# Kernel tuning notes

Hardware: AMD Instinct MI355X
Metric: run time of the kernel (lower is better)

## Reference

```python
import jax, jax.numpy as jnp
import numpy as np

B, IN_DIM, HID, S = 131072, 8, 32, 16
ERR_THR = 0.01          # QuantumErrorCorrection.error_threshold
ENT_STRENGTH = 0.4      # config.quantum_entanglement_strength
EULER_DT = 0.1


def setup_inputs() -> dict:
    key = jax.random.key(0)
    ks = jax.random.split(key, 7)
    x = jax.random.normal(ks[0], (B, IN_DIM), dtype=jnp.float32)
    h_quantum = jax.random.normal(ks[1], (B, HID, S), dtype=jnp.float32)
    quantum_weights = jax.random.normal(ks[2], (IN_DIM, HID, S), dtype=jnp.float32) * 0.1
    recurrent_weights = jax.random.normal(ks[3], (HID, HID, S), dtype=jnp.float32) * 0.1
    base_tau = jax.random.uniform(ks[4], (HID,), dtype=jnp.float32, minval=1.0, maxval=50.0)
    syndrome_matrix = jax.random.normal(ks[5], (4, S), dtype=jnp.float32)
    correction_weights = jax.random.normal(ks[6], (4, S), dtype=jnp.float32) * 0.1
    return {"x": x, "h_quantum": h_quantum, "quantum_weights": quantum_weights,
            "recurrent_weights": recurrent_weights, "base_tau": base_tau,
            "syndrome_matrix": syndrome_matrix, "correction_weights": correction_weights}


def reference(x, h_quantum, quantum_weights, recurrent_weights, base_tau,
              syndrome_matrix, correction_weights):
    # --- quantum error correction (thresholded syndrome correction) ---
    # syndrome: [B, H, C]
    syndrome = jnp.einsum('bhs,cs->bhc', h_quantum, syndrome_matrix)
    masked_syndrome = jnp.where(jnp.abs(syndrome) > ERR_THR, syndrome, 0.0)
    h_q = h_quantum - jnp.einsum('bhc,cs->bhs', masked_syndrome, correction_weights)

    # --- liquid ODE update, fused over all superposition states ---
    # adaptation_factor = 1.0 (OPTIMAL health, no performance stats)
    tau = base_tau[None, :, None]                              # [1, H, 1]
    inp = jnp.einsum('bi,ihs->bhs', x, quantum_weights)        # [B, H, S]
    rec = jnp.einsum('bhs,hks->bks', h_q, recurrent_weights)   # [B, H, S]
    activation = jnp.tanh(inp + rec)                           # no fault detected -> tanh path
    new_q = h_q + EULER_DT * (-h_q / tau + activation)

    # --- nearest-neighbor entanglement between adjacent states ---
    coupling = ENT_STRENGTH * new_q[:, :, :-1] * new_q[:, :, 1:]       # [B, H, S-1]
    ent = (jnp.pad(coupling, ((0, 0), (0, 0), (0, 1)))
           + jnp.pad(coupling, ((0, 0), (0, 0), (1, 0))))
    stable = new_q + 0.1 * ent
    norms = jnp.linalg.norm(stable, axis=1, keepdims=True)             # [B, 1, S]
    q_norm = stable / (norms + 1e-8)

    # --- adaptive measurement (QUANTUM_OPTIMIZED -> balanced branch) ---
    energy = jnp.sum(q_norm ** 2, axis=1, keepdims=True)               # [B, 1, S]
    magnitude = jnp.sum(jnp.abs(q_norm), axis=1, keepdims=True)        # [B, 1, S]
    probs = magnitude / (energy + 1e-6)
    probs = probs / jnp.sum(probs, axis=-1, keepdims=True)
    output = jnp.sum(q_norm * probs, axis=-1)                          # [B, H]
    return (output, q_norm)
```

## Files before the change

### kernel.cpp

```cpp
#include <hip/hip_runtime.h>

typedef __attribute__((ext_vector_type(8))) __bf16 bf16x8;
typedef __attribute__((ext_vector_type(8))) unsigned short us8;
typedef __attribute__((ext_vector_type(4))) float f32x4;

#define NB 16
#define B_TOTAL 131072

__device__ __forceinline__ unsigned short f2bf(float f) {
  union { float f; unsigned int u; } c; c.f = f;
  unsigned int u = c.u;
  u += 0x7fffu + ((u >> 16) & 1u);
  return (unsigned short)(u >> 16);
}
__device__ __forceinline__ float bf2f(unsigned short s) {
  union { unsigned int u; float f; } c; c.u = ((unsigned int)s) << 16;
  return c.f;
}
__device__ __forceinline__ bf16x8 as_bf(us8 v) {
  union { us8 u; bf16x8 b; } c; c.u = v; return c.b;
}
__device__ __forceinline__ float fast_tanh(float x) {
  float t = __expf(2.0f * x);
  return 1.0f - 2.0f / (t + 1.0f);
}

__global__ void shq_prep(const float* __restrict__ qw, const float* __restrict__ rw,
                         const float* __restrict__ tau,
                         unsigned short* __restrict__ rwfrag,
                         unsigned short* __restrict__ qwfrag,
                         unsigned short* __restrict__ dgfrag) {
  int g = blockIdx.x * 256 + threadIdx.x;
  if (g < 2048) {
    int s = g >> 7, kh = (g >> 6) & 1, ln = g & 63;
    int k = kh * 16 + (ln & 15), h0 = (ln >> 4) * 8;
    us8 v;
#pragma unroll
    for (int e = 0; e < 8; ++e) v[e] = f2bf(rw[((h0 + e) * 32 + k) * 16 + s]);
    *(us8*)(rwfrag + g * 8) = v;
  } else if (g < 2560) {
    int j = g - 2048;
    int s = j >> 5, kh = (j >> 4) & 1, ln = j & 15;
    int hc = kh * 16 + ln;
    us8 v;
#pragma unroll
    for (int e = 0; e < 8; ++e) v[e] = f2bf(qw[(e * 32 + hc) * 16 + s]);
    *(us8*)(qwfrag + j * 8) = v;
  } else if (g < 2688) {
    int j = g - 2560;
    int kh = (j >> 6) & 1, ln = j & 63;
    int k = kh * 16 + (ln & 15), h0 = (ln >> 4) * 8;
    unsigned short ab = f2bf(1.0f - 0.1f / tau[k]);
    us8 v;
#pragma unroll
    for (int e = 0; e < 8; ++e) v[e] = (h0 + e == k) ? ab : (unsigned short)0;
    *(us8*)(dgfrag + j * 8) = v;
  }
}

__global__ __launch_bounds__(512, 4) void shq_main(
    const float* __restrict__ x, const float* __restrict__ hq_g,
    const float* __restrict__ syn, const float* __restrict__ corr,
    const unsigned short* __restrict__ rwfrag,
    const unsigned short* __restrict__ qwfrag,
    const unsigned short* __restrict__ dgfrag,
    float* __restrict__ out) {
  __shared__ unsigned short lds_a[10368];
  __shared__ unsigned short lds_nq[10368];
  __shared__ float lds_pi[NB * 16 * 2];

  const int tid = threadIdx.x;
  const int b0 = blockIdx.x * NB;
  const int lane = tid & 63;
  const int w = tid >> 6;

  us8 z8 = {0, 0, 0, 0, 0, 0, 0, 0};
  us8 rwf_[2][2], qwf_[2][2], dg_[2];
#pragma unroll
  for (int sl = 0; sl < 2; ++sl) {
#pragma unroll
    for (int kh = 0; kh < 2; ++kh) {
      int s = 2 * w + sl;
      rwf_[sl][kh] = *(const us8*)(rwfrag + ((s * 2 + kh) * 64 + lane) * 8);
      qwf_[sl][kh] = (lane < 16) ? *(const us8*)(qwfrag + ((s * 2 + kh) * 16 + lane) * 8) : z8;
    }
  }
  dg_[0] = *(const us8*)(dgfrag + lane * 8);
  dg_[1] = *(const us8*)(dgfrag + (64 + lane) * 8);
  us8 xu = z8;
  if (lane < 16) {
    const float* xb = x + (size_t)(b0 + lane) * 8;
    f32x4 a = *(const f32x4*)xb, b = *(const f32x4*)(xb + 4);
    xu[0] = f2bf(a[0]); xu[1] = f2bf(a[1]); xu[2] = f2bf(a[2]); xu[3] = f2bf(a[3]);
    xu[4] = f2bf(b[0]); xu[5] = f2bf(b[1]); xu[6] = f2bf(b[2]); xu[7] = f2bf(b[3]);
  }

  {
    const int bl = tid >> 5, hh = tid & 31;
    const float* hb = hq_g + (((size_t)(b0 + bl) * 32) + hh) * 16;
    f32x4 h0 = *(const f32x4*)(hb), h1 = *(const f32x4*)(hb + 4);
    f32x4 h2 = *(const f32x4*)(hb + 8), h3 = *(const f32x4*)(hb + 12);
    float hrow[16];
#pragma unroll
    for (int q = 0; q < 4; ++q) {
      hrow[0 + q] = h0[q]; hrow[4 + q] = h1[q]; hrow[8 + q] = h2[q]; hrow[12 + q] = h3[q];
    }
    float sd[4];
#pragma unroll
    for (int c = 0; c < 4; ++c) {
      float a = 0.f;
#pragma unroll
      for (int s = 0; s < 16; ++s) a = fmaf(hrow[s], syn[c * 16 + s], a);
      sd[c] = (fabsf(a) > 0.01f) ? a : 0.f;
    }
#pragma unroll
    for (int s = 0; s < 16; ++s) {
      float cs = sd[0] * corr[s] + sd[1] * corr[16 + s] + sd[2] * corr[32 + s] + sd[3] * corr[48 + s];
      lds_a[s * 640 + bl * 40 + hh] = f2bf(hrow[s] - cs);
    }
  }
  __syncthreads();

  {
    f32x4 zro = {0.f, 0.f, 0.f, 0.f};
#pragma unroll
    for (int sl = 0; sl < 2; ++sl) {
      int s = 2 * w + sl;
      us8 hq_u = *(const us8*)&lds_a[s * 640 + (lane & 15) * 40 + (lane >> 4) * 8];
      bf16x8 hqf = as_bf(hq_u);
#pragma unroll
      for (int kh = 0; kh < 2; ++kh) {
        f32x4 acc = __builtin_amdgcn_mfma_f32_16x16x32_bf16(as_bf(xu), as_bf(qwf_[sl][kh]), zro, 0, 0, 0);
        acc = __builtin_amdgcn_mfma_f32_16x16x32_bf16(hqf, as_bf(rwf_[sl][kh]), acc, 0, 0, 0);
        f32x4 na;
#pragma unroll
        for (int r = 0; r < 4; ++r) na[r] = 0.1f * fast_tanh(acc[r]);
        na = __builtin_amdgcn_mfma_f32_16x16x32_bf16(hqf, as_bf(dg_[kh]), na, 0, 0, 0);
#pragma unroll
        for (int r = 0; r < 4; ++r) {
          int br = (lane >> 4) * 4 + r;
          int k = kh * 16 + (lane & 15);
          lds_nq[br * 648 + s * 40 + k] = f2bf(na[r]);
        }
      }
    }
  }
  __syncthreads();

  if (tid < 256) {
    int b3 = tid >> 4, s3 = tid & 15;
    int base = b3 * 648 + s3 * 40;
    us8 r0[4], rm[4], rp[4];
#pragma unroll
    for (int q = 0; q < 4; ++q) {
      r0[q] = *(const us8*)&lds_nq[base + q * 8];
      rm[q] = (s3 > 0) ? *(const us8*)&lds_nq[base - 40 + q * 8] : z8;
      rp[q] = (s3 < 15) ? *(const us8*)&lds_nq[base + 40 + q * 8] : z8;
    }
    float ssq = 0.f, sab = 0.f;
#pragma unroll
    for (int q = 0; q < 4; ++q) {
      us8 stq;
#pragma unroll
      for (int e = 0; e < 8; ++e) {
        float n0 = bf2f(r0[q][e]);
        float ent = 0.4f * n0 * bf2f(rp[q][e]) + 0.4f * bf2f(rm[q][e]) * n0;
        float st = fmaf(0.1f, ent, n0);
        ssq = fmaf(st, st, ssq);
        sab += fabsf(st);
        stq[e] = f2bf(st);
      }
      *(us8*)&lds_a[base + q * 8] = stq;
    }
    float norm = sqrtf(ssq);
    float inv = 1.0f / (norm + 1e-8f);
    float energy = ssq * inv * inv;
    float mag = sab * inv;
    float pu = mag / (energy + 1e-6f);
    float psum = pu;
#pragma unroll
    for (int m = 1; m < 16; m <<= 1) psum += __shfl_xor(psum, m, 16);
    lds_pi[(b3 * 16 + s3) * 2 + 0] = pu / psum;
    lds_pi[(b3 * 16 + s3) * 2 + 1] = inv;
  }
  __syncthreads();

  {
    const int b3 = tid >> 5, h3 = tid & 31;
    float oacc = 0.f;
    float qn[16];
#pragma unroll
    for (int s = 0; s < 16; ++s) {
      float st = bf2f(lds_a[b3 * 648 + s * 40 + h3]);
      float2 pi = *(const float2*)&lds_pi[(b3 * 16 + s) * 2];
      float q = st * pi.y;
      qn[s] = q;
      oacc = fmaf(q, pi.x, oacc);
    }
    out[(size_t)(b0 + b3) * 32 + h3] = oacc;
    float* qp = out + 4194304 + (((size_t)(b0 + b3) * 32) + h3) * 16;
    f32x4 q0 = {qn[0], qn[1], qn[2], qn[3]};
    f32x4 q1 = {qn[4], qn[5], qn[6], qn[7]};
    f32x4 q2 = {qn[8], qn[9], qn[10], qn[11]};
    f32x4 q3 = {qn[12], qn[13], qn[14], qn[15]};
    *(f32x4*)(qp) = q0; *(f32x4*)(qp + 4) = q1;
    *(f32x4*)(qp + 8) = q2; *(f32x4*)(qp + 12) = q3;
  }
}

extern "C" void kernel_launch(void* const* d_in, const int* in_sizes, int n_in,
                              void* d_out, int out_size, void* d_ws, size_t ws_size,
                              hipStream_t stream) {
  const float* x    = (const float*)d_in[0];
  const float* hq   = (const float*)d_in[1];
  const float* qw   = (const float*)d_in[2];
  const float* rw   = (const float*)d_in[3];
  const float* tau  = (const float*)d_in[4];
  const float* syn  = (const float*)d_in[5];
  const float* corr = (const float*)d_in[6];
  unsigned short* ws = (unsigned short*)d_ws;
  unsigned short* rwfrag = ws;
  unsigned short* qwfrag = ws + 16384;
  unsigned short* dgfrag = ws + 20480;
  shq_prep<<<11, 256, 0, stream>>>(qw, rw, tau, rwfrag, qwfrag, dgfrag);
  shq_main<<<B_TOTAL / NB, 512, 0, stream>>>(x, hq, syn, corr, rwfrag, qwfrag, dgfrag, (float*)d_out);
}
```

Baseline: 154.1 us.

## Share one fp32 LDS buffer, defer weight loads, recompute entanglement, raise occupancy

Replaces the two bf16 LDS buffers with a single fp32 buffer that is reused: first for the transposed corrected state, then for the ODE result kept in fp32. Weight fragments are loaded just before use rather than held in registers for the whole kernel, and launch bounds now ask for 8 waves per SIMD. The stabilised values are no longer written back to LDS; the final stage recomputes the neighbour coupling from the fp32 column. Fast divides replace precise ones. The aim is lower LDS and register use for higher occupancy, at the cost of an extra barrier, some recomputation, and a risk of register spills under the tighter bound.

New measurement: 287.8 us. +86.8%, slower.

```diff
diff --git a/kernel.cpp b/kernel.cpp
--- a/kernel.cpp
+++ b/kernel.cpp
@@ -6,16 +6,14 @@
 
 #define NB 16
 #define B_TOTAL 131072
+#define SST 36
+#define BST 580
 
 __device__ __forceinline__ unsigned short f2bf(float f) {
   union { float f; unsigned int u; } c; c.f = f;
   unsigned int u = c.u;
   u += 0x7fffu + ((u >> 16) & 1u);
   return (unsigned short)(u >> 16);
-}
-__device__ __forceinline__ float bf2f(unsigned short s) {
-  union { unsigned int u; float f; } c; c.u = ((unsigned int)s) << 16;
-  return c.f;
 }
 __device__ __forceinline__ bf16x8 as_bf(us8 v) {
   union { us8 u; bf16x8 b; } c; c.u = v; return c.b;
@@ -58,16 +56,16 @@
   }
 }
 
-__global__ __launch_bounds__(512, 4) void shq_main(
+__global__ __launch_bounds__(512, 8) void shq_main(
     const float* __restrict__ x, const float* __restrict__ hq_g,
     const float* __restrict__ syn, const float* __restrict__ corr,
     const unsigned short* __restrict__ rwfrag,
     const unsigned short* __restrict__ qwfrag,
     const unsigned short* __restrict__ dgfrag,
     float* __restrict__ out) {
-  __shared__ unsigned short lds_a[10368];
-  __shared__ unsigned short lds_nq[10368];
+  __shared__ float smem[16 * BST];
   __shared__ float lds_pi[NB * 16 * 2];
+  unsigned short* hqT = (unsigned short*)smem;
 
   const int tid = threadIdx.x;
   const int b0 = blockIdx.x * NB;
@@ -75,18 +73,7 @@
   const int w = tid >> 6;
 
   us8 z8 = {0, 0, 0, 0, 0, 0, 0, 0};
-  us8 rwf_[2][2], qwf_[2][2], dg_[2];
-#pragma unroll
-  for (int sl = 0; sl < 2; ++sl) {
-#pragma unroll
-    for (int kh = 0; kh < 2; ++kh) {
-      int s = 2 * w + sl;
-      rwf_[sl][kh] = *(const us8*)(rwfrag + ((s * 2 + kh) * 64 + lane) * 8);
-      qwf_[sl][kh] = (lane < 16) ? *(const us8*)(qwfrag + ((s * 2 + kh) * 16 + lane) * 8) : z8;
-    }
-  }
-  dg_[0] = *(const us8*)(dgfrag + lane * 8);
-  dg_[1] = *(const us8*)(dgfrag + (64 + lane) * 8);
+
   us8 xu = z8;
   if (lane < 16) {
     const float* xb = x + (size_t)(b0 + lane) * 8;
@@ -94,6 +81,8 @@
     xu[0] = f2bf(a[0]); xu[1] = f2bf(a[1]); xu[2] = f2bf(a[2]); xu[3] = f2bf(a[3]);
     xu[4] = f2bf(b[0]); xu[5] = f2bf(b[1]); xu[6] = f2bf(b[2]); xu[7] = f2bf(b[3]);
   }
+  us8 dg0 = *(const us8*)(dgfrag + lane * 8);
+  us8 dg1 = *(const us8*)(dgfrag + (64 + lane) * 8);
 
   {
     const int bl = tid >> 5, hh = tid & 31;
@@ -116,9 +105,15 @@
 #pragma unroll
     for (int s = 0; s < 16; ++s) {
       float cs = sd[0] * corr[s] + sd[1] * corr[16 + s] + sd[2] * corr[32 + s] + sd[3] * corr[48 + s];
-      lds_a[s * 640 + bl * 40 + hh] = f2bf(hrow[s] - cs);
-    }
-  }
+      hqT[s * 640 + bl * 40 + hh] = f2bf(hrow[s] - cs);
+    }
+  }
+  __syncthreads();
+
+  us8 hq_u[2];
+#pragma unroll
+  for (int sl = 0; sl < 2; ++sl)
+    hq_u[sl] = *(const us8*)&hqT[(2 * w + sl) * 640 + (lane & 15) * 40 + (lane >> 4) * 8];
   __syncthreads();
 
   {
@@ -126,21 +121,24 @@
 #pragma unroll
     for (int sl = 0; sl < 2; ++sl) {
       int s = 2 * w + sl;
-      us8 hq_u = *(const us8*)&lds_a[s * 640 + (lane & 15) * 40 + (lane >> 4) * 8];
-      bf16x8 hqf = as_bf(hq_u);
+      us8 rw0 = *(const us8*)(rwfrag + ((s * 2 + 0) * 64 + lane) * 8);
+      us8 rw1 = *(const us8*)(rwfrag + ((s * 2 + 1) * 64 + lane) * 8);
+      us8 qw0 = (lane < 16) ? *(const us8*)(qwfrag + ((s * 2 + 0) * 16 + lane) * 8) : z8;
+      us8 qw1 = (lane < 16) ? *(const us8*)(qwfrag + ((s * 2 + 1) * 16 + lane) * 8) : z8;
+      bf16x8 hqf = as_bf(hq_u[sl]);
 #pragma unroll
       for (int kh = 0; kh < 2; ++kh) {
-        f32x4 acc = __builtin_amdgcn_mfma_f32_16x16x32_bf16(as_bf(xu), as_bf(qwf_[sl][kh]), zro, 0, 0, 0);
-        acc = __builtin_amdgcn_mfma_f32_16x16x32_bf16(hqf, as_bf(rwf_[sl][kh]), acc, 0, 0, 0);
+        f32x4 acc = __builtin_amdgcn_mfma_f32_16x16x32_bf16(as_bf(xu), as_bf(kh ? qw1 : qw0), zro, 0, 0, 0);
+        acc = __builtin_amdgcn_mfma_f32_16x16x32_bf16(hqf, as_bf(kh ? rw1 : rw0), acc, 0, 0, 0);
         f32x4 na;
 #pragma unroll
         for (int r = 0; r < 4; ++r) na[r] = 0.1f * fast_tanh(acc[r]);
-        na = __builtin_amdgcn_mfma_f32_16x16x32_bf16(hqf, as_bf(dg_[kh]), na, 0, 0, 0);
+        na = __builtin_amdgcn_mfma_f32_16x16x32_bf16(hqf, as_bf(kh ? dg1 : dg0), na, 0, 0, 0);
+        int k = kh * 16 + (lane & 15);
 #pragma unroll
         for (int r = 0; r < 4; ++r) {
           int br = (lane >> 4) * 4 + r;
-          int k = kh * 16 + (lane & 15);
-          lds_nq[br * 648 + s * 40 + k] = f2bf(na[r]);
+          smem[br * BST + s * SST + k] = na[r];
         }
       }
     }
@@ -149,53 +147,51 @@
 
   if (tid < 256) {
     int b3 = tid >> 4, s3 = tid & 15;
-    int base = b3 * 648 + s3 * 40;
-    us8 r0[4], rm[4], rp[4];
-#pragma unroll
-    for (int q = 0; q < 4; ++q) {
-      r0[q] = *(const us8*)&lds_nq[base + q * 8];
-      rm[q] = (s3 > 0) ? *(const us8*)&lds_nq[base - 40 + q * 8] : z8;
-      rp[q] = (s3 < 15) ? *(const us8*)&lds_nq[base + 40 + q * 8] : z8;
-    }
+    int base = b3 * BST + s3 * SST;
     float ssq = 0.f, sab = 0.f;
-#pragma unroll
-    for (int q = 0; q < 4; ++q) {
-      us8 stq;
-#pragma unroll
-      for (int e = 0; e < 8; ++e) {
-        float n0 = bf2f(r0[q][e]);
-        float ent = 0.4f * n0 * bf2f(rp[q][e]) + 0.4f * bf2f(rm[q][e]) * n0;
-        float st = fmaf(0.1f, ent, n0);
+    f32x4 zv = {0.f, 0.f, 0.f, 0.f};
+#pragma unroll
+    for (int q = 0; q < 8; ++q) {
+      f32x4 c0 = *(const f32x4*)&smem[base + 4 * q];
+      f32x4 cm = (s3 > 0)  ? *(const f32x4*)&smem[base - SST + 4 * q] : zv;
+      f32x4 cp = (s3 < 15) ? *(const f32x4*)&smem[base + SST + 4 * q] : zv;
+#pragma unroll
+      for (int e = 0; e < 4; ++e) {
+        float st = fmaf(0.04f * c0[e], cm[e] + cp[e], c0[e]);
         ssq = fmaf(st, st, ssq);
         sab += fabsf(st);
-        stq[e] = f2bf(st);
       }
-      *(us8*)&lds_a[base + q * 8] = stq;
-    }
-    float norm = sqrtf(ssq);
-    float inv = 1.0f / (norm + 1e-8f);
+    }
+    float inv = __fdividef(1.0f, sqrtf(ssq) + 1e-8f);
     float energy = ssq * inv * inv;
     float mag = sab * inv;
-    float pu = mag / (energy + 1e-6f);
+    float pu = __fdividef(mag, energy + 1e-6f);
     float psum = pu;
 #pragma unroll
     for (int m = 1; m < 16; m <<= 1) psum += __shfl_xor(psum, m, 16);
-    lds_pi[(b3 * 16 + s3) * 2 + 0] = pu / psum;
+    lds_pi[(b3 * 16 + s3) * 2 + 0] = __fdividef(pu, psum);
     lds_pi[(b3 * 16 + s3) * 2 + 1] = inv;
   }
   __syncthreads();
 
   {
     const int b3 = tid >> 5, h3 = tid & 31;
+    float col[16];
+#pragma unroll
+    for (int s = 0; s < 16; ++s) col[s] = smem[b3 * BST + s * SST + h3];
+    float cc[15];
+#pragma unroll
+    for (int s = 0; s < 15; ++s) cc[s] = 0.4f * col[s] * col[s + 1];
     float oacc = 0.f;
     float qn[16];
 #pragma unroll
     for (int s = 0; s < 16; ++s) {
-      float st = bf2f(lds_a[b3 * 648 + s * 40 + h3]);
-      float2 pi = *(const float2*)&lds_pi[(b3 * 16 + s) * 2];
-      float q = st * pi.y;
+      float ent = ((s > 0) ? cc[s - 1] : 0.f) + ((s < 15) ? cc[s] : 0.f);
+      float st = fmaf(0.1f, ent, col[s]);
+      float2 pv = *(const float2*)&lds_pi[(b3 * 16 + s) * 2];
+      float q = st * pv.y;
       qn[s] = q;
-      oacc = fmaf(q, pi.x, oacc);
+      oacc = fmaf(q, pv.x, oacc);
     }
     out[(size_t)(b0 + b3) * 32 + h3] = oacc;
     float* qp = out + 4194304 + (((size_t)(b0 + b3) * 32) + h3) * 16;
```
